# Kernel tuning notes

Hardware: AMD Instinct MI355X
Metric: run time of the kernel (lower is better)

## Reference

```python
import jax, jax.numpy as jnp
import numpy as np

N_STARS = 4096
N_DIC = 4096
N_FEAT = 16  # (d_max+1)(d_max+2)/2 + graph_features = 10 + 6
OPD_DIM = 256
BATCH = 2048


def setup_inputs() -> dict:
    key = jax.random.key(0)
    k1, k2, k3, k4, k5 = jax.random.split(key, 5)
    # Observed star positions in the FoV (x_lims/y_lims = [0, 4096]).
    obs_pos = jax.random.uniform(k1, (N_STARS, 2), dtype=jnp.float32) * 4096.0
    # Query positions MUST be exact rows of obs_pos (the layer does an
    # exact-equality search); take a random subset of stars.
    perm = jax.random.permutation(k2, N_STARS)[:BATCH]
    positions = obs_pos[perm]
    spatial_dic = jax.random.normal(k3, (N_STARS, N_DIC), dtype=jnp.float32)
    alpha_mat = jax.random.normal(k4, (N_DIC, N_FEAT), dtype=jnp.float32)
    # S initialized uniform in [-1e-3, 1e-3] in the original layer.
    S_mat = (jax.random.uniform(k5, (N_FEAT, OPD_DIM, OPD_DIM), dtype=jnp.float32) * 2.0 - 1.0) * 1e-3
    return {
        "positions": positions,
        "obs_pos": obs_pos,
        "spatial_dic": spatial_dic,
        "alpha_mat": alpha_mat,
        "S_mat": S_mat,
    }


def _lookup_indices(positions, obs_pos):
    # Faithful to tf.where(tf.equal(obs_pos, pos))[0, 0]: elementwise equality
    # against the full (n_stars, 2) table, take the row of the FIRST matching
    # element in row-major order.
    eq = positions[:, None, :] == obs_pos[None, :, :]          # [batch, n_stars, 2]
    flat = eq.reshape(eq.shape[0], -1)                          # [batch, n_stars*2]
    first = jnp.argmax(flat, axis=1)                            # first True, row-major
    return first // 2                                           # row index -> int


def reference(positions, obs_pos, spatial_dic, alpha_mat, S_mat):
    indices = _lookup_indices(positions, obs_pos)               # [batch]
    batch_dict = jnp.take(spatial_dic, indices, axis=0)         # [batch, n_dic]
    inter = batch_dict @ alpha_mat                              # [batch, n_feat]
    # tensordot over the feature axis -> [batch, opd_dim, opd_dim]
    return jnp.einsum("bf,fij->bij", inter, S_mat)
```

## Files before the change

kernel.cpp:

```cpp
#include <hip/hip_runtime.h>
#include <cstdint>

#define NSTARS 4096
#define NDIC   4096
#define NFEAT  16
#define NPIX   65536
#define BATCH  2048
#define BPB    128

using f32x4 = __attribute__((ext_vector_type(4))) float;

__global__ __launch_bounds__(256) void k_inter(
    const float*  __restrict__ positions,
    const float2* __restrict__ obs,
    const float*  __restrict__ spatial,
    const float*  __restrict__ alpha,
    float*        __restrict__ inter)
{
    __shared__ int   s_idx[4];
    __shared__ float s_red[4 * 64];

    const int tid = threadIdx.x;
    const int b0  = blockIdx.x * 4;

    if (tid < 4) s_idx[tid] = 0x7FFFFFFF;
    __syncthreads();

    float px[4], py[4];
    #pragma unroll
    for (int b = 0; b < 4; ++b) {
        px[b] = positions[(b0 + b) * 2 + 0];
        py[b] = positions[(b0 + b) * 2 + 1];
    }

    for (int s = tid; s < NSTARS; s += 256) {
        float2 o = obs[s];
        #pragma unroll
        for (int b = 0; b < 4; ++b) {
            if (px[b] == o.x || py[b] == o.y) atomicMin(&s_idx[b], s);
        }
    }
    __syncthreads();

    int idx[4];
    #pragma unroll
    for (int b = 0; b < 4; ++b) {
        int v = s_idx[b];
        idx[b] = (v == 0x7FFFFFFF) ? 0 : v;
    }

    float acc[4][NFEAT];
    #pragma unroll
    for (int b = 0; b < 4; ++b)
        #pragma unroll
        for (int f = 0; f < NFEAT; ++f) acc[b][f] = 0.0f;

    const float4* alpha4 = (const float4*)alpha;

    #pragma unroll
    for (int step = 0; step < 4; ++step) {
        const int d0 = tid * 4 + step * 1024;
        float4 v[4];
        #pragma unroll
        for (int b = 0; b < 4; ++b)
            v[b] = *(const float4*)(spatial + (size_t)idx[b] * NDIC + d0);

        #pragma unroll
        for (int k = 0; k < 4; ++k) {
            const float4 a0 = alpha4[(size_t)(d0 + k) * 4 + 0];
            const float4 a1 = alpha4[(size_t)(d0 + k) * 4 + 1];
            const float4 a2 = alpha4[(size_t)(d0 + k) * 4 + 2];
            const float4 a3 = alpha4[(size_t)(d0 + k) * 4 + 3];
            #pragma unroll
            for (int b = 0; b < 4; ++b) {
                const float vb = (&v[b].x)[k];
                acc[b][0]  += vb * a0.x;  acc[b][1]  += vb * a0.y;
                acc[b][2]  += vb * a0.z;  acc[b][3]  += vb * a0.w;
                acc[b][4]  += vb * a1.x;  acc[b][5]  += vb * a1.y;
                acc[b][6]  += vb * a1.z;  acc[b][7]  += vb * a1.w;
                acc[b][8]  += vb * a2.x;  acc[b][9]  += vb * a2.y;
                acc[b][10] += vb * a2.z;  acc[b][11] += vb * a2.w;
                acc[b][12] += vb * a3.x;  acc[b][13] += vb * a3.y;
                acc[b][14] += vb * a3.z;  acc[b][15] += vb * a3.w;
            }
        }
    }

    #pragma unroll
    for (int b = 0; b < 4; ++b)
        #pragma unroll
        for (int f = 0; f < NFEAT; ++f) {
            float x = acc[b][f];
            #pragma unroll
            for (int off = 32; off > 0; off >>= 1)
                x += __shfl_down(x, off);
            acc[b][f] = x;
        }

    const int lane = tid & 63;
    const int wave = tid >> 6;
    if (lane == 0) {
        #pragma unroll
        for (int b = 0; b < 4; ++b)
            #pragma unroll
            for (int f = 0; f < NFEAT; ++f)
                s_red[wave * 64 + b * NFEAT + f] = acc[b][f];
    }
    __syncthreads();

    if (tid < 64) {
        const int b = tid >> 4, f = tid & 15;
        float x = s_red[0 * 64 + tid] + s_red[1 * 64 + tid]
                + s_red[2 * 64 + tid] + s_red[3 * 64 + tid];
        inter[(size_t)(b0 + b) * NFEAT + f] = x;
    }
}

__global__ __launch_bounds__(256) void k_opd(
    const float4* __restrict__ inter4,
    const f32x4*  __restrict__ S4,
    f32x4*        __restrict__ out4)
{
    const int tid   = threadIdx.x;
    const int chunk = blockIdx.x & 63;
    const int bg    = blockIdx.x >> 6;
    const int p4    = chunk * 256 + tid;

    f32x4 s[NFEAT];
    #pragma unroll
    for (int f = 0; f < NFEAT; ++f)
        s[f] = S4[(size_t)f * (NPIX / 4) + p4];

    const float4* w4 = inter4 + (size_t)bg * BPB * 4;
    f32x4* o = out4 + (size_t)bg * BPB * (NPIX / 4) + p4;

    #pragma unroll 2
    for (int b = 0; b < BPB; ++b) {
        const float4 wa = w4[b * 4 + 0];
        const float4 wb = w4[b * 4 + 1];
        const float4 wc = w4[b * 4 + 2];
        const float4 wd = w4[b * 4 + 3];

        f32x4 acc = s[0] * wa.x;
        acc += s[1]  * wa.y;  acc += s[2]  * wa.z;  acc += s[3]  * wa.w;
        acc += s[4]  * wb.x;  acc += s[5]  * wb.y;  acc += s[6]  * wb.z;
        acc += s[7]  * wb.w;  acc += s[8]  * wc.x;  acc += s[9]  * wc.y;
        acc += s[10] * wc.z;  acc += s[11] * wc.w;  acc += s[12] * wd.x;
        acc += s[13] * wd.y;  acc += s[14] * wd.z;  acc += s[15] * wd.w;

        __builtin_nontemporal_store(acc, o + (size_t)b * (NPIX / 4));
    }
}

extern "C" void kernel_launch(void* const* d_in, const int* in_sizes, int n_in,
                              void* d_out, int out_size, void* d_ws, size_t ws_size,
                              hipStream_t stream) {
    const float*  positions = (const float*)d_in[0];
    const float2* obs       = (const float2*)d_in[1];
    const float*  spatial   = (const float*)d_in[2];
    const float*  alpha     = (const float*)d_in[3];
    const f32x4*  S4        = (const f32x4*)d_in[4];
    f32x4*        out       = (f32x4*)d_out;
    float*        inter     = (float*)d_ws;

    k_inter<<<BATCH / 4, 256, 0, stream>>>(positions, obs, spatial, alpha, inter);
    k_opd<<<(NPIX / 1024) * (BATCH / BPB), 256, 0, stream>>>(
        (const float4*)inter, S4, out);
}
```

Before: 146.0 us.

## Split inter computation across dictionary segments with one wave per batch row

```diff
diff --git a/kernel.cpp b/kernel.cpp
--- a/kernel.cpp
+++ b/kernel.cpp
@@ -7,6 +7,7 @@
 #define NPIX   65536
 #define BATCH  2048
 #define BPB    128
+#define NSEG   4
 
 using f32x4 = __attribute__((ext_vector_type(4))) float;
 
@@ -15,13 +16,16 @@
     const float2* __restrict__ obs,
     const float*  __restrict__ spatial,
     const float*  __restrict__ alpha,
-    float*        __restrict__ inter)
+    float*        __restrict__ partial)
 {
-    __shared__ int   s_idx[4];
-    __shared__ float s_red[4 * 64];
+    __shared__ int s_idx[4];
 
-    const int tid = threadIdx.x;
-    const int b0  = blockIdx.x * 4;
+    const int tid  = threadIdx.x;
+    const int seg  = blockIdx.x & (NSEG - 1);
+    const int q    = blockIdx.x >> 2;
+    const int wave = tid >> 6;
+    const int lane = tid & 63;
+    const int b0   = q * 4;
 
     if (tid < 4) s_idx[tid] = 0x7FFFFFFF;
     __syncthreads();
@@ -32,7 +36,6 @@
         px[b] = positions[(b0 + b) * 2 + 0];
         py[b] = positions[(b0 + b) * 2 + 1];
     }
-
     for (int s = tid; s < NSTARS; s += 256) {
         float2 o = obs[s];
         #pragma unroll
@@ -42,84 +45,58 @@
     }
     __syncthreads();
 
-    int idx[4];
+    int v = s_idx[wave];
+    const int idx = (v == 0x7FFFFFFF) ? 0 : v;
+    const int row = b0 + wave;
+
+    const float*  srow   = spatial + (size_t)idx * NDIC + seg * 1024;
+    const float4* alpha4 = (const float4*)alpha + (size_t)seg * 1024 * 4;
+
+    float acc[NFEAT];
     #pragma unroll
-    for (int b = 0; b < 4; ++b) {
-        int v = s_idx[b];
-        idx[b] = (v == 0x7FFFFFFF) ? 0 : v;
-    }
-
-    float acc[4][NFEAT];
-    #pragma unroll
-    for (int b = 0; b < 4; ++b)
-        #pragma unroll
-        for (int f = 0; f < NFEAT; ++f) acc[b][f] = 0.0f;
-
-    const float4* alpha4 = (const float4*)alpha;
+    for (int f = 0; f < NFEAT; ++f) acc[f] = 0.0f;
 
     #pragma unroll
-    for (int step = 0; step < 4; ++step) {
-        const int d0 = tid * 4 + step * 1024;
-        float4 v[4];
-        #pragma unroll
-        for (int b = 0; b < 4; ++b)
-            v[b] = *(const float4*)(spatial + (size_t)idx[b] * NDIC + d0);
-
+    for (int pass = 0; pass < 4; ++pass) {
+        const int d = pass * 256 + lane * 4;
+        const float4 vv = *(const float4*)(srow + d);
         #pragma unroll
         for (int k = 0; k < 4; ++k) {
-            const float4 a0 = alpha4[(size_t)(d0 + k) * 4 + 0];
-            const float4 a1 = alpha4[(size_t)(d0 + k) * 4 + 1];
-            const float4 a2 = alpha4[(size_t)(d0 + k) * 4 + 2];
-            const float4 a3 = alpha4[(size_t)(d0 + k) * 4 + 3];
-            #pragma unroll
-            for (int b = 0; b < 4; ++b) {
-                const float vb = (&v[b].x)[k];
-                acc[b][0]  += vb * a0.x;  acc[b][1]  += vb * a0.y;
-                acc[b][2]  += vb * a0.z;  acc[b][3]  += vb * a0.w;
-                acc[b][4]  += vb * a1.x;  acc[b][5]  += vb * a1.y;
-                acc[b][6]  += vb * a1.z;  acc[b][7]  += vb * a1.w;
-                acc[b][8]  += vb * a2.x;  acc[b][9]  += vb * a2.y;
-                acc[b][10] += vb * a2.z;  acc[b][11] += vb * a2.w;
-                acc[b][12] += vb * a3.x;  acc[b][13] += vb * a3.y;
-                acc[b][14] += vb * a3.z;  acc[b][15] += vb * a3.w;
-            }
+            const float4 a0 = alpha4[(size_t)(d + k) * 4 + 0];
+            const float4 a1 = alpha4[(size_t)(d + k) * 4 + 1];
+            const float4 a2 = alpha4[(size_t)(d + k) * 4 + 2];
+            const float4 a3 = alpha4[(size_t)(d + k) * 4 + 3];
+            const float vb = (&vv.x)[k];
+            acc[0]  += vb * a0.x;  acc[1]  += vb * a0.y;
+            acc[2]  += vb * a0.z;  acc[3]  += vb * a0.w;
+            acc[4]  += vb * a1.x;  acc[5]  += vb * a1.y;
+            acc[6]  += vb * a1.z;  acc[7]  += vb * a1.w;
+            acc[8]  += vb * a2.x;  acc[9]  += vb * a2.y;
+            acc[10] += vb * a2.z;  acc[11] += vb * a2.w;
+            acc[12] += vb * a3.x;  acc[13] += vb * a3.y;
+            acc[14] += vb * a3.z;  acc[15] += vb * a3.w;
         }
     }
 
     #pragma unroll
-    for (int b = 0; b < 4; ++b)
+    for (int off = 1; off < 64; off <<= 1)
         #pragma unroll
-        for (int f = 0; f < NFEAT; ++f) {
-            float x = acc[b][f];
-            #pragma unroll
-            for (int off = 32; off > 0; off >>= 1)
-                x += __shfl_down(x, off);
-            acc[b][f] = x;
-        }
+        for (int f = 0; f < NFEAT; ++f)
+            acc[f] += __shfl_xor(acc[f], off);
 
-    const int lane = tid & 63;
-    const int wave = tid >> 6;
     if (lane == 0) {
-        #pragma unroll
-        for (int b = 0; b < 4; ++b)
-            #pragma unroll
-            for (int f = 0; f < NFEAT; ++f)
-                s_red[wave * 64 + b * NFEAT + f] = acc[b][f];
-    }
-    __syncthreads();
-
-    if (tid < 64) {
-        const int b = tid >> 4, f = tid & 15;
-        float x = s_red[0 * 64 + tid] + s_red[1 * 64 + tid]
-                + s_red[2 * 64 + tid] + s_red[3 * 64 + tid];
-        inter[(size_t)(b0 + b) * NFEAT + f] = x;
+        float* p = partial + ((size_t)seg * BATCH + row) * NFEAT;
+        *(float4*)(p + 0)  = make_float4(acc[0],  acc[1],  acc[2],  acc[3]);
+        *(float4*)(p + 4)  = make_float4(acc[4],  acc[5],  acc[6],  acc[7]);
+        *(float4*)(p + 8)  = make_float4(acc[8],  acc[9],  acc[10], acc[11]);
+        *(float4*)(p + 12) = make_float4(acc[12], acc[13], acc[14], acc[15]);
     }
 }
 
 __global__ __launch_bounds__(256) void k_opd(
-    const float4* __restrict__ inter4,
-    const f32x4*  __restrict__ S4,
-    f32x4*        __restrict__ out4)
+    const f32x4* __restrict__ part4,
+    const f32x4* __restrict__ S4,
+    f32x4*       __restrict__ out4)
 {
     const int tid   = threadIdx.x;
     const int chunk = blockIdx.x & 63;
@@ -131,15 +108,19 @@
     for (int f = 0; f < NFEAT; ++f)
         s[f] = S4[(size_t)f * (NPIX / 4) + p4];
 
-    const float4* w4 = inter4 + (size_t)bg * BPB * 4;
     f32x4* o = out4 + (size_t)bg * BPB * (NPIX / 4) + p4;
 
     #pragma unroll 2
     for (int b = 0; b < BPB; ++b) {
-        const float4 wa = w4[b * 4 + 0];
-        const float4 wb = w4[b * 4 + 1];
-        const float4 wc = w4[b * 4 + 2];
-        const float4 wd = w4[b * 4 + 3];
+        const size_t bi = (size_t)bg * BPB + b;
+        const f32x4 wa = part4[(0 * BATCH + bi) * 4 + 0] + part4[(1 * BATCH + bi) * 4 + 0]
+                       + part4[(2 * BATCH + bi) * 4 + 0] + part4[(3 * BATCH + bi) * 4 + 0];
+        const f32x4 wb = part4[(0 * BATCH + bi) * 4 + 1] + part4[(1 * BATCH + bi) * 4 + 1]
+                       + part4[(2 * BATCH + bi) * 4 + 1] + part4[(3 * BATCH + bi) * 4 + 1];
+        const f32x4 wc = part4[(0 * BATCH + bi) * 4 + 2] + part4[(1 * BATCH + bi) * 4 + 2]
+                       + part4[(2 * BATCH + bi) * 4 + 2] + part4[(3 * BATCH + bi) * 4 + 2];
+        const f32x4 wd = part4[(0 * BATCH + bi) * 4 + 3] + part4[(1 * BATCH + bi) * 4 + 3]
+                       + part4[(2 * BATCH + bi) * 4 + 3] + part4[(3 * BATCH + bi) * 4 + 3];
 
         f32x4 acc = s[0] * wa.x;
         acc += s[1]  * wa.y;  acc += s[2]  * wa.z;  acc += s[3]  * wa.w;
@@ -161,9 +142,9 @@
     const float*  alpha     = (const float*)d_in[3];
     const f32x4*  S4        = (const f32x4*)d_in[4];
     f32x4*        out       = (f32x4*)d_out;
-    float*        inter     = (float*)d_ws;
+    float*        partial   = (float*)d_ws;
 
-    k_inter<<<BATCH / 4, 256, 0, stream>>>(positions, obs, spatial, alpha, inter);
+    k_inter<<<512 * NSEG, 256, 0, stream>>>(positions, obs, spatial, alpha, partial);
     k_opd<<<(NPIX / 1024) * (BATCH / BPB), 256, 0, stream>>>(
-        (const float4*)inter, S4, out);
+        (const f32x4*)partial, S4, out);
 }
```

After: 175.7 us. 20.3% more time.
